# Kernel tuning notes

Measured on AMD Instinct MI355X. Metric: run time of the kernel, lower is better.

The kernel has to match this reference:

```python
import jax, jax.numpy as jnp
import numpy as np

L, H, DH, D, F, V, ENC, PAST = 8, 8, 128, 1024, 4096, 16384, 438, 447
MAXPOS = PAST + 1


def _ln(x, g, b):
    m = jnp.mean(x, -1, keepdims=True)
    v = jnp.mean((x - m) ** 2, -1, keepdims=True)
    return (x - m) * jax.lax.rsqrt(v + 1e-5) * g + b


def setup_inputs() -> dict:
    key = jax.random.key(0)
    ks = jax.random.split(key, 30)
    rn = lambda k, shape: jax.random.normal(k, shape, jnp.float32) * 0.02
    inp = {
        'input_ids': jax.random.randint(ks[0], (1, 1), 0, V, jnp.int32),
        'encoder_hidden_states': jax.random.normal(ks[1], (1, ENC, D), jnp.float32),
        'past_k': jax.random.normal(ks[2], (L, 1, H, PAST, DH), jnp.float32),
        'past_v': jax.random.normal(ks[3], (L, 1, H, PAST, DH), jnp.float32),
        'emb': rn(ks[4], (V, D)),
        'pos': rn(ks[5], (MAXPOS, D)),
        'ln1_g': jnp.ones((L, D), jnp.float32), 'ln1_b': jnp.zeros((L, D), jnp.float32),
        'wq_s': rn(ks[6], (L, D, D)), 'wk_s': rn(ks[7], (L, D, D)),
        'wv_s': rn(ks[8], (L, D, D)), 'wo_s': rn(ks[9], (L, D, D)),
        'ln2_g': jnp.ones((L, D), jnp.float32), 'ln2_b': jnp.zeros((L, D), jnp.float32),
        'wq_c': rn(ks[10], (L, D, D)), 'wk_c': rn(ks[11], (L, D, D)),
        'wv_c': rn(ks[12], (L, D, D)), 'wo_c': rn(ks[13], (L, D, D)),
        'ln3_g': jnp.ones((L, D), jnp.float32), 'ln3_b': jnp.zeros((L, D), jnp.float32),
        'w1': rn(ks[14], (L, D, F)), 'w2': rn(ks[15], (L, F, D)),
        'lnf_g': jnp.ones((D,), jnp.float32), 'lnf_b': jnp.zeros((D,), jnp.float32),
        'past_length': PAST,
    }
    return inp


def reference(input_ids, encoder_hidden_states, past_k, past_v, emb, pos,
              ln1_g, ln1_b, wq_s, wk_s, wv_s, wo_s,
              ln2_g, ln2_b, wq_c, wk_c, wv_c, wo_c,
              ln3_g, ln3_b, w1, w2, lnf_g, lnf_b, past_length):
    scale = 1.0 / np.sqrt(DH)
    # token embedding + learned position embedding at the current position
    x = emb[input_ids] + pos[past_length][None, None, :]  # (1,1,D)
    heads1 = lambda t: t.reshape(1, 1, H, DH).transpose(0, 2, 1, 3)      # (1,H,1,dh)
    for l in range(L):
        # --- self-attention over cached K/V + new token (pre-LN) ---
        h = _ln(x, ln1_g[l], ln1_b[l])
        q = heads1(h @ wq_s[l])
        k = heads1(h @ wk_s[l])
        v = heads1(h @ wv_s[l])
        K = jnp.concatenate([past_k[l], k], axis=2)   # (1,H,PAST+1,dh)
        Vv = jnp.concatenate([past_v[l], v], axis=2)
        a = jax.nn.softmax(jnp.einsum('bhqd,bhkd->bhqk', q, K) * scale, axis=-1)
        o = jnp.einsum('bhqk,bhkd->bhqd', a, Vv).transpose(0, 2, 1, 3).reshape(1, 1, D)
        x = x + o @ wo_s[l]
        # --- cross-attention to encoder states ---
        h = _ln(x, ln2_g[l], ln2_b[l])
        q = heads1(h @ wq_c[l])
        Kc = (encoder_hidden_states @ wk_c[l]).reshape(1, ENC, H, DH).transpose(0, 2, 1, 3)
        Vc = (encoder_hidden_states @ wv_c[l]).reshape(1, ENC, H, DH).transpose(0, 2, 1, 3)
        a = jax.nn.softmax(jnp.einsum('bhqd,bhkd->bhqk', q, Kc) * scale, axis=-1)
        o = jnp.einsum('bhqk,bhkd->bhqd', a, Vc).transpose(0, 2, 1, 3).reshape(1, 1, D)
        x = x + o @ wo_c[l]
        # --- FFN ---
        h = _ln(x, ln3_g[l], ln3_b[l])
        x = x + jax.nn.gelu(h @ w1[l]) @ w2[l]
    x = _ln(x, lnf_g, lnf_b)
    logits = x @ emb.T  # tied lm_head -> (1,1,V)
    return logits
```

## Files before the change

kernel.cpp:

```cpp
#include <hip/hip_runtime.h>
#include <hip/hip_bf16.h>

#define D 1024
#define Hh 8
#define DHd 128
#define Ff 4096
#define Ll 8
#define Vv 16384
#define ENCn 438
#define PASTn 447
#define NCH 7
#define SCALE 0.08838834764831845f

typedef __hip_bfloat16 bf16;
typedef __attribute__((ext_vector_type(8))) short short8;
typedef __attribute__((ext_vector_type(4))) float floatx4;

template<typename T> __device__ __forceinline__ float ldg_(const void* p, size_t i);
template<> __device__ __forceinline__ float ldg_<bf16>(const void* p, size_t i) {
    return __bfloat162float(((const bf16*)p)[i]);
}
template<> __device__ __forceinline__ float ldg_<float>(const void* p, size_t i) {
    return ((const float*)p)[i];
}
template<typename T> __device__ __forceinline__ void stg_(void* p, size_t i, float v);
template<> __device__ __forceinline__ void stg_<bf16>(void* p, size_t i, float v) {
    ((bf16*)p)[i] = __float2bfloat16(v);
}
template<> __device__ __forceinline__ void stg_<float>(void* p, size_t i, float v) {
    ((float*)p)[i] = v;
}

template<typename T> __device__ __forceinline__ void load8(const void* p, size_t i, float* o);
template<> __device__ __forceinline__ void load8<bf16>(const void* p, size_t i, float* o) {
    short8 v = *reinterpret_cast<const short8*>(reinterpret_cast<const short*>(p) + i);
#pragma unroll
    for (int k = 0; k < 8; k++)
        o[k] = __uint_as_float(((unsigned)(unsigned short)v[k]) << 16);
}
template<> __device__ __forceinline__ void load8<float>(const void* p, size_t i, float* o) {
    const floatx4* q = reinterpret_cast<const floatx4*>(reinterpret_cast<const float*>(p) + i);
    floatx4 a = q[0], b = q[1];
#pragma unroll
    for (int k = 0; k < 4; k++) { o[k] = a[k]; o[4 + k] = b[k]; }
}

__device__ __forceinline__ float blkmax(float v, float* sm) {
#pragma unroll
    for (int off = 32; off; off >>= 1) v = fmaxf(v, __shfl_xor(v, off));
    __syncthreads();
    if ((threadIdx.x & 63) == 0) sm[threadIdx.x >> 6] = v;
    __syncthreads();
    return fmaxf(fmaxf(sm[0], sm[1]), fmaxf(sm[2], sm[3]));
}
__device__ __forceinline__ float blksum(float v, float* sm) {
#pragma unroll
    for (int off = 32; off; off >>= 1) v += __shfl_xor(v, off);
    __syncthreads();
    if ((threadIdx.x & 63) == 0) sm[threadIdx.x >> 6] = v;
    __syncthreads();
    return sm[0] + sm[1] + sm[2] + sm[3];
}
__device__ __forceinline__ void blksum2(float a, float b, float* sm, float& oa, float& ob) {
#pragma unroll
    for (int off = 32; off; off >>= 1) { a += __shfl_xor(a, off); b += __shfl_xor(b, off); }
    __syncthreads();
    if ((threadIdx.x & 63) == 0) { int w = threadIdx.x >> 6; sm[w] = a; sm[4 + w] = b; }
    __syncthreads();
    oa = sm[0] + sm[1] + sm[2] + sm[3];
    ob = sm[4] + sm[5] + sm[6] + sm[7];
}

__device__ __forceinline__ float comb4(const float* P, int i) {
    return P[i] + P[1024 + i] + P[2048 + i] + P[3072 + i];
}

template<typename T, int NROWS>
__device__ __forceinline__ float mv_tile(const void* W, size_t base, int ldW,
                                         const float* xs, float* sm) {
    int c8 = threadIdx.x & 7, s = threadIdx.x >> 3;
    const int IT = NROWS / 32;
    float acc[8];
#pragma unroll
    for (int k = 0; k < 8; k++) acc[k] = 0.f;
    size_t idx = base + (size_t)(s * IT) * ldW + c8 * 8;
#pragma unroll 8
    for (int it = 0; it < IT; ++it) {
        float w8[8];
        load8<T>(W, idx, w8);
        float xv = xs[s * IT + it];
#pragma unroll
        for (int k = 0; k < 8; k++) acc[k] = fmaf(xv, w8[k], acc[k]);
        idx += (size_t)ldW;
    }
    __syncthreads();
#pragma unroll
    for (int k = 0; k < 8; k++) sm[s * 64 + c8 * 8 + k] = acc[k];
    __syncthreads();
    float y = 0.f;
    if (threadIdx.x < 64) {
#pragma unroll 8
        for (int s2 = 0; s2 < 32; s2++) y += sm[s2 * 64 + threadIdx.x];
    }
    return y;
}

template<typename T>
__device__ __forceinline__ void ln_slice(const float* Xp, const void* g, const void* b,
                                         size_t o1, int row0, float* xs, float* sm) {
    int t = threadIdx.x;
    float xv[4];
    float s = 0.f, sq = 0.f;
#pragma unroll
    for (int k = 0; k < 4; k++) {
        float v = comb4(Xp, t * 4 + k);
        xv[k] = v; s += v; sq += v * v;
    }
    float S, SQ;
    blksum2(s, sq, sm, S, SQ);
    float m = S * (1.f / D);
    float rstd = rsqrtf(SQ * (1.f / D) - m * m + 1e-5f);
#pragma unroll
    for (int k = 0; k < 4; k++) {
        int i = t * 4 + k;
        int rel = i - row0;
        if ((unsigned)rel < 256u)
            xs[rel] = (xv[k] - m) * rstd * ldg_<T>(g, o1 + i) + ldg_<T>(b, o1 + i);
    }
    __syncthreads();
}

__global__ void k_probe(const void* ones, int* flag) {
    if (threadIdx.x == 0)
        *flag = (*(const unsigned*)ones == 0x3F803F80u) ? 1 : 0;
}

template<typename T>
__device__ void embed_body(const int* ids, const int* plen, const void* emb,
                           const void* pos, float* XAp) {
    int t = threadIdx.x;
    int id = ids[0], pl = plen[0];
    for (int i = t; i < D; i += 256) {
        XAp[i] = ldg_<T>(emb, (size_t)id * D + i) + ldg_<T>(pos, (size_t)pl * D + i);
        XAp[1024 + i] = 0.f; XAp[2048 + i] = 0.f; XAp[3072 + i] = 0.f;
    }
}
__global__ __launch_bounds__(256) void k_embed(const int* flag, const int* ids,
                                               const int* plen, const void* emb,
                                               const void* pos, float* XAp) {
    if (*flag) embed_body<bf16>(ids, plen, emb, pos, XAp);
    else       embed_body<float>(ids, plen, emb, pos, XAp);
}

template<typename T>
__device__ void qkv_body(const float* XAp, const void* g, const void* b, size_t o1,
                         const void* W0, const void* W1, const void* W2, size_t o2,
                         float* qp, float* kp, float* vp, float* xs, float* sm) {
    int bid = blockIdx.x;
    int mat = bid >> 6, rem = bid & 63;
    int cb = rem >> 2, rc = rem & 3;
    int j0 = cb * 64, row0 = rc * 256;
    ln_slice<T>(XAp, g, b, o1, row0, xs, sm);
    const void* W = (mat == 0) ? W0 : ((mat == 1) ? W1 : W2);
    float* out = (mat == 0) ? qp : ((mat == 1) ? kp : vp);
    float y = mv_tile<T, 256>(W, o2 + (size_t)row0 * D + j0, D, xs, sm);
    if (threadIdx.x < 64) out[rc * 1024 + j0 + threadIdx.x] = y;
}
__global__ __launch_bounds__(256) void k_qkv(const int* flag,
    const float* XAp, const void* g, const void* b, size_t o1,
    const void* W0, const void* W1, const void* W2, size_t o2,
    float* qp, float* kp, float* vp) {
    __shared__ float xs[256];
    __shared__ float sm[2048];
    if (*flag) qkv_body<bf16>(XAp, g, b, o1, W0, W1, W2, o2, qp, kp, vp, xs, sm);
    else       qkv_body<float>(XAp, g, b, o1, W0, W1, W2, o2, qp, kp, vp, xs, sm);
}

template<typename T>
__device__ void attn_body(const float* qp, const float* kp, const float* vp,
                          const void* pk, const void* pv, size_t kvo,
                          float* pm, float* plv, float* pacc,
                          float* qsh, float* knl, float* vnl, float* sc, float* sm) {
    int h = blockIdx.x / NCH, cc = blockIdx.x % NCH;
    int t = threadIdx.x;
    if (t < 128) {
        qsh[t] = comb4(qp, h * 128 + t);
        if (cc == NCH - 1) vnl[t] = comb4(vp, h * 128 + t);
    } else if (cc == NCH - 1) {
        int d = t - 128;
        knl[d] = comb4(kp, h * 128 + d);
    }
    __syncthreads();
    int kk = t >> 2, part = t & 3;
    int p = cc * 64 + kk;
    float acc = 0.f;
    if (p < PASTn) {
        size_t base = kvo + ((size_t)h * PASTn + p) * DHd + part * 32;
#pragma unroll
        for (int w = 0; w < 4; w++) {
            float k8[8]; load8<T>(pk, base + w * 8, k8);
#pragma unroll
            for (int j = 0; j < 8; j++) acc = fmaf(qsh[part * 32 + w * 8 + j], k8[j], acc);
        }
    } else {
#pragma unroll 8
        for (int j = 0; j < 32; j++) acc += qsh[part * 32 + j] * knl[part * 32 + j];
    }
    acc += __shfl_xor(acc, 1);
    acc += __shfl_xor(acc, 2);
    if (part == 0) sc[kk] = acc * SCALE;
    __syncthreads();
    float v0 = (t < 64) ? sc[t] : -1e30f;
    float M = blkmax(v0, sm);
    float e = (t < 64) ? expf(sc[t] - M) : 0.f;
    if (t < 64) sc[t] = e;
    float lsum = blksum(e, sm);
    int dv = t & 15, kg = t >> 4;
    float a8[8];
#pragma unroll
    for (int k = 0; k < 8; k++) a8[k] = 0.f;
#pragma unroll
    for (int q4 = 0; q4 < 4; q4++) {
        int k2 = kg + q4 * 16;
        int p2 = cc * 64 + k2;
        float pw = sc[k2];
        if (p2 < PASTn) {
            float v8[8];
            load8<T>(pv, kvo + ((size_t)h * PASTn + p2) * DHd + dv * 8, v8);
#pragma unroll
            for (int j = 0; j < 8; j++) a8[j] = fmaf(pw, v8[j], a8[j]);
        } else {
#pragma unroll
            for (int j = 0; j < 8; j++) a8[j] = fmaf(pw, vnl[dv * 8 + j], a8[j]);
        }
    }
    __syncthreads();
#pragma unroll
    for (int j = 0; j < 8; j++) sm[kg * 128 + dv * 8 + j] = a8[j];
    __syncthreads();
    if (t < 128) {
        float s = 0.f;
#pragma unroll 4
        for (int g2 = 0; g2 < 16; g2++) s += sm[g2 * 128 + t];
        pacc[((size_t)h * NCH + cc) * 128 + t] = s;
    }
    if (t == 0) { pm[h * 8 + cc] = M; plv[h * 8 + cc] = lsum; }
}
__global__ __launch_bounds__(256) void k_attn(const int* flag,
    const float* qp, const float* kp, const float* vp,
    const void* pk, const void* pv, size_t kvo,
    float* pm, float* plv, float* pacc) {
    __shared__ float qsh[128], knl[128], vnl[128], sc[64];
    __shared__ float sm[2048];
    if (*flag) attn_body<bf16>(qp, kp, vp, pk, pv, kvo, pm, plv, pacc, qsh, knl, vnl, sc, sm);
    else       attn_body<float>(qp, kp, vp, pk, pv, kvo, pm, plv, pacc, qsh, knl, vnl, sc, sm);
}

template<typename T>
__device__ void combwo_body(const float* pm, const float* plv, const float* pacc,
                            const void* W, size_t o2, const float* XAp, float* XBp,
                            float* fac, float* xs, float* sm) {
    int cb = blockIdx.x >> 2, rc = blockIdx.x & 3;
    int j0 = cb * 64, row0 = rc * 256;
    int t = threadIdx.x;
    if (t < Hh) {
        float M = -1e30f;
        for (int c = 0; c < NCH; c++) M = fmaxf(M, pm[t * 8 + c]);
        float fs[NCH]; float den = 0.f;
        for (int c = 0; c < NCH; c++) { fs[c] = expf(pm[t * 8 + c] - M); den += fs[c] * plv[t * 8 + c]; }
        float inv = 1.f / den;
        for (int c = 0; c < NCH; c++) fac[t * NCH + c] = fs[c] * inv;
    }
    __syncthreads();
    int hd = row0 + t;
    int h = hd >> 7, d = hd & 127;
    float o = 0.f;
#pragma unroll
    for (int c = 0; c < NCH; c++) o += fac[h * NCH + c] * pacc[((size_t)h * NCH + c) * 128 + d];
    xs[t] = o;
    __syncthreads();
    float y = mv_tile<T, 256>(W, o2 + (size_t)row0 * D + j0, D, xs, sm);
    if (t < 64) {
        float r = (rc == 0) ? comb4(XAp, j0 + t) : 0.f;
        XBp[rc * 1024 + j0 + t] = y + r;
    }
}
__global__ __launch_bounds__(256) void k_combwo(const int* flag,
    const float* pm, const float* plv, const float* pacc,
    const void* W, size_t o2, const float* XAp, float* XBp) {
    __shared__ float fac[Hh * NCH];
    __shared__ float xs[256];
    __shared__ float sm[2048];
    if (*flag) combwo_body<bf16>(pm, plv, pacc, W, o2, XAp, XBp, fac, xs, sm);
    else       combwo_body<float>(pm, plv, pacc, W, o2, XAp, XBp, fac, xs, sm);
}

template<typename T>
__device__ void lnmv_body(const float* Xp, const void* g, const void* b, size_t o1,
                          const void* W, size_t wo, int ldW, float* outp,
                          float* xs, float* sm) {
    int cb = blockIdx.x >> 2, rc = blockIdx.x & 3;
    int j0 = cb * 64, row0 = rc * 256;
    ln_slice<T>(Xp, g, b, o1, row0, xs, sm);
    float y = mv_tile<T, 256>(W, wo + (size_t)row0 * ldW + j0, ldW, xs, sm);
    if (threadIdx.x < 64) outp[(size_t)rc * ldW + j0 + threadIdx.x] = y;
}
__global__ __launch_bounds__(256) void k_lnmv(const int* flag,
    const float* Xp, const void* g, const void* b, size_t o1,
    const void* W, size_t wo, int ldW, float* outp) {
    __shared__ float xs[256];
    __shared__ float sm[2048];
    if (*flag) lnmv_body<bf16>(Xp, g, b, o1, W, wo, ldW, outp, xs, sm);
    else       lnmv_body<float>(Xp, g, b, o1, W, wo, ldW, outp, xs, sm);
}

template<typename T>
__device__ void tvec_body(const float* qcp, const void* Wk, size_t o2, float* tv, float* qsl) {
    int h = blockIdx.x >> 3, dc = blockIdx.x & 7;
    int t = threadIdx.x;
    if (t < 128) qsl[t] = comb4(qcp, h * 128 + t);
    __syncthreads();
    int out = t >> 1, half = t & 1;
    int d = dc * 128 + out;
    size_t base = o2 + (size_t)d * D + h * 128 + half * 64;
    float acc = 0.f;
#pragma unroll
    for (int w = 0; w < 8; w++) {
        float w8[8]; load8<T>(Wk, base + w * 8, w8);
#pragma unroll
        for (int j = 0; j < 8; j++) acc = fmaf(qsl[half * 64 + w * 8 + j], w8[j], acc);
    }
    acc += __shfl_xor(acc, 1);
    if (half == 0) tv[(size_t)h * D + d] = acc * SCALE;
}
__global__ __launch_bounds__(256) void k_tvec(const int* flag, const float* qcp,
                                              const void* Wk, size_t o2, float* tv) {
    __shared__ float qsl[128];
    if (*flag) tvec_body<bf16>(qcp, Wk, o2, tv, qsl);
    else       tvec_body<float>(qcp, Wk, o2, tv, qsl);
}

template<typename T>
__device__ void cscore_body(const void* enc, const float* tv, float* scb, float* tsh) {
    int h = blockIdx.x / 14, rcw = blockIdx.x % 14;
    int t = threadIdx.x;
#pragma unroll
    for (int k = 0; k < 4; k++) tsh[t * 4 + k] = tv[(size_t)h * D + t * 4 + k];
    __syncthreads();
    int rr = t >> 3, part = t & 7;
    int r = rcw * 32 + rr;
    float acc = 0.f;
    if (r < ENCn) {
        size_t base = (size_t)r * D + part * 128;
#pragma unroll 8
        for (int w = 0; w < 16; w++) {
            float e8[8]; load8<T>(enc, base + w * 8, e8);
#pragma unroll
            for (int j = 0; j < 8; j++) acc = fmaf(tsh[part * 128 + w * 8 + j], e8[j], acc);
        }
    }
    acc += __shfl_xor(acc, 1);
    acc += __shfl_xor(acc, 2);
    acc += __shfl_xor(acc, 4);
    if (part == 0 && r < ENCn) scb[h * 448 + r] = acc;
}
__global__ __launch_bounds__(256) void k_cscore(const int* flag, const void* enc,
                                                const float* tv, float* scb) {
    __shared__ float tsh[D];
    if (*flag) cscore_body<bf16>(enc, tv, scb, tsh);
    else       cscore_body<float>(enc, tv, scb, tsh);
}

template<typename T>
__device__ void softw_body(const float* scb, const void* enc, float* wvb,
                           float* p, float* sm) {
    int h = blockIdx.x >> 3, dc = blockIdx.x & 7;
    int t = threadIdx.x;
    float v1 = (t < ENCn) ? scb[h * 448 + t] : -1e30f;
    float v2 = (256 + t < ENCn) ? scb[h * 448 + 256 + t] : -1e30f;
    float M = blkmax(fmaxf(v1, v2), sm);
    float e1 = (t < ENCn) ? expf(v1 - M) : 0.f;
    float e2 = (256 + t < ENCn) ? expf(v2 - M) : 0.f;
    p[t] = e1;
    if (t + 256 < 448) p[t + 256] = e2;
    float inv = 1.f / blksum(e1 + e2, sm);
    int dv = t & 15, rg = t >> 4;
    float a8[8];
#pragma unroll
    for (int k = 0; k < 8; k++) a8[k] = 0.f;
    for (int r = rg; r < ENCn; r += 16) {
        float e8[8]; load8<T>(enc, (size_t)r * D + dc * 128 + dv * 8, e8);
        float pw = p[r];
#pragma unroll
        for (int j = 0; j < 8; j++) a8[j] = fmaf(pw, e8[j], a8[j]);
    }
    __syncthreads();
#pragma unroll
    for (int j = 0; j < 8; j++) sm[rg * 128 + dv * 8 + j] = a8[j];
    __syncthreads();
    if (t < 128) {
        float s = 0.f;
#pragma unroll 4
        for (int g2 = 0; g2 < 16; g2++) s += sm[g2 * 128 + t];
        wvb[(size_t)h * D + dc * 128 + t] = s * inv;
    }
}
__global__ __launch_bounds__(256) void k_softw(const int* flag, const float* scb,
                                               const void* enc, float* wvb) {
    __shared__ float p[448];
    __shared__ float sm[2048];
    if (*flag) softw_body<bf16>(scb, enc, wvb, p, sm);
    else       softw_body<float>(scb, enc, wvb, p, sm);
}

template<typename T>
__device__ void ovec_body(const float* wvb, const void* Wv, size_t o2, float* ocp,
                          float* xs, float* sm) {
    int cb = blockIdx.x >> 2, rc = blockIdx.x & 3;
    int j0 = cb * 64, row0 = rc * 256;
    int h = j0 >> 7;
    int t = threadIdx.x;
    xs[t] = wvb[(size_t)h * D + row0 + t];
    __syncthreads();
    float y = mv_tile<T, 256>(Wv, o2 + (size_t)row0 * D + j0, D, xs, sm);
    if (t < 64) ocp[rc * 1024 + j0 + t] = y;
}
__global__ __launch_bounds__(256) void k_ovec(const int* flag, const float* wvb,
                                              const void* Wv, size_t o2, float* ocp) {
    __shared__ float xs[256];
    __shared__ float sm[2048];
    if (*flag) ovec_body<bf16>(wvb, Wv, o2, ocp, xs, sm);
    else       ovec_body<float>(wvb, Wv, o2, ocp, xs, sm);
}

template<typename T>
__device__ void woc_body(const float* ocp, const void* W, size_t o2,
                         const float* XBp, float* XCp, float* xs, float* sm) {
    int cb = blockIdx.x >> 2, rc = blockIdx.x & 3;
    int j0 = cb * 64, row0 = rc * 256;
    int t = threadIdx.x;
    xs[t] = comb4(ocp, row0 + t);
    __syncthreads();
    float y = mv_tile<T, 256>(W, o2 + (size_t)row0 * D + j0, D, xs, sm);
    if (t < 64) {
        float r = (rc == 0) ? comb4(XBp, j0 + t) : 0.f;
        XCp[rc * 1024 + j0 + t] = y + r;
    }
}
__global__ __launch_bounds__(256) void k_woc(const int* flag, const float* ocp,
    const void* W, size_t o2, const float* XBp, float* XCp) {
    __shared__ float xs[256];
    __shared__ float sm[2048];
    if (*flag) woc_body<bf16>(ocp, W, o2, XBp, XCp, xs, sm);
    else       woc_body<float>(ocp, W, o2, XBp, XCp, xs, sm);
}

template<typename T>
__device__ void w2_body(const float* ubp, const void* W, size_t oG,
                        const float* XCp, float* XAp, float* xs, float* sm) {
    int cb = blockIdx.x >> 2, rc = blockIdx.x & 3;
    int j0 = cb * 64, row0 = rc * 1024;
    int t = threadIdx.x;
#pragma unroll
    for (int k = 0; k < 4; k++) {
        int i = t * 4 + k;
        int gi = row0 + i;
        float u = ubp[gi] + ubp[4096 + gi] + ubp[8192 + gi] + ubp[12288 + gi];
        float g2 = 0.7978845608028654f * (u + 0.044715f * u * u * u);
        xs[i] = 0.5f * u * (1.f + tanhf(g2));
    }
    __syncthreads();
    float y = mv_tile<T, 1024>(W, oG + (size_t)row0 * D + j0, D, xs, sm);
    if (t < 64) {
        float r = (rc == 0) ? comb4(XCp, j0 + t) : 0.f;
        XAp[rc * 1024 + j0 + t] = y + r;
    }
}
__global__ __launch_bounds__(256) void k_w2(const int* flag, const float* ubp,
    const void* W, size_t oG, const float* XCp, float* XAp) {
    __shared__ float xs[1024];
    __shared__ float sm[2048];
    if (*flag) w2_body<bf16>(ubp, W, oG, XCp, XAp, xs, sm);
    else       w2_body<float>(ubp, W, oG, XCp, XAp, xs, sm);
}

template<typename T>
__device__ void logits_body(const float* XAp, const void* g, const void* b,
                            const void* emb, void* out, float* hsh, float* sm) {
    int t = threadIdx.x;
    float xv[4];
    float s = 0.f, sq = 0.f;
#pragma unroll
    for (int k = 0; k < 4; k++) {
        float v = comb4(XAp, t * 4 + k);
        xv[k] = v; s += v; sq += v * v;
    }
    float S, SQ;
    blksum2(s, sq, sm, S, SQ);
    float m = S * (1.f / D);
    float rstd = rsqrtf(SQ * (1.f / D) - m * m + 1e-5f);
#pragma unroll
    for (int k = 0; k < 4; k++) {
        int i = t * 4 + k;
        hsh[i] = (xv[k] - m) * rstd * ldg_<T>(g, i) + ldg_<T>(b, i);
    }
    __syncthreads();
    int v = blockIdx.x * 64 + (t >> 2), part = t & 3;
    size_t base = (size_t)v * D + part * 256;
    float acc = 0.f;
#pragma unroll 8
    for (int w = 0; w < 32; w++) {
        float e8[8]; load8<T>(emb, base + w * 8, e8);
#pragma unroll
        for (int j = 0; j < 8; j++) acc = fmaf(hsh[part * 256 + w * 8 + j], e8[j], acc);
    }
    acc += __shfl_xor(acc, 1);
    acc += __shfl_xor(acc, 2);
    if (part == 0) stg_<T>(out, v, acc);
}
__global__ __launch_bounds__(256) void k_logits(const int* flag, const float* XAp,
                                                const void* g, const void* b,
                                                const void* emb, void* out) {
    __shared__ float hsh[D];
    __shared__ float sm[8];
    if (*flag) logits_body<bf16>(XAp, g, b, emb, out, hsh, sm);
    else       logits_body<float>(XAp, g, b, emb, out, hsh, sm);
}

extern "C" void kernel_launch(void* const* d_in, const int* in_sizes, int n_in,
                              void* d_out, int out_size, void* d_ws, size_t ws_size,
                              hipStream_t stream) {
    const int*  ids    = (const int*)d_in[0];
    const void* enc    = d_in[1];
    const void* past_k = d_in[2];
    const void* past_v = d_in[3];
    const void* emb    = d_in[4];
    const void* pos    = d_in[5];
    const void* ln1_g  = d_in[6];
    const void* ln1_b  = d_in[7];
    const void* wq_s   = d_in[8];
    const void* wk_s   = d_in[9];
    const void* wv_s   = d_in[10];
    const void* wo_s   = d_in[11];
    const void* ln2_g  = d_in[12];
    const void* ln2_b  = d_in[13];
    const void* wq_c   = d_in[14];
    const void* wk_c   = d_in[15];
    const void* wv_c   = d_in[16];
    const void* wo_c   = d_in[17];
    const void* ln3_g  = d_in[18];
    const void* ln3_b  = d_in[19];
    const void* w1     = d_in[20];
    const void* w2     = d_in[21];
    const void* lnf_g  = d_in[22];
    const void* lnf_b  = d_in[23];
    const int*  plen   = (const int*)d_in[24];

    float* ws   = (float*)d_ws;
    float* XAp  = ws;
    float* XBp  = ws + 4096;
    float* XCp  = ws + 8192;
    float* qp   = ws + 12288;
    float* kp   = ws + 16384;
    float* vp   = ws + 20480;
    float* qcp  = ws + 24576;
    float* ocp  = ws + 28672;
    float* pm   = ws + 32768;
    float* plv  = ws + 32832;
    float* pacc = ws + 32896;
    float* tv   = ws + 40064;
    float* scb  = ws + 48256;
    float* wvb  = ws + 51840;
    float* ubp  = ws + 60032;
    int*   flag = (int*)(ws + 76416);

    k_probe<<<1, 64, 0, stream>>>(ln1_g, flag);
    k_embed<<<1, 256, 0, stream>>>(flag, ids, plen, emb, pos, XAp);

    for (int l = 0; l < Ll; l++) {
        size_t o1  = (size_t)l * D;
        size_t o2  = (size_t)l * D * D;
        size_t oF  = (size_t)l * D * Ff;
        size_t oG  = (size_t)l * Ff * D;
        size_t oKV = (size_t)l * Hh * PASTn * DHd;

        k_qkv<<<192, 256, 0, stream>>>(flag, XAp, ln1_g, ln1_b, o1,
                                       wq_s, wk_s, wv_s, o2, qp, kp, vp);
        k_attn<<<56, 256, 0, stream>>>(flag, qp, kp, vp, past_k, past_v, oKV,
                                       pm, plv, pacc);
        k_combwo<<<64, 256, 0, stream>>>(flag, pm, plv, pacc, wo_s, o2, XAp, XBp);
        k_lnmv<<<64, 256, 0, stream>>>(flag, XBp, ln2_g, ln2_b, o1,
                                       wq_c, o2, D, qcp);
        k_tvec<<<64, 256, 0, stream>>>(flag, qcp, wk_c, o2, tv);
        k_cscore<<<112, 256, 0, stream>>>(flag, enc, tv, scb);
        k_softw<<<64, 256, 0, stream>>>(flag, scb, enc, wvb);
        k_ovec<<<64, 256, 0, stream>>>(flag, wvb, wv_c, o2, ocp);
        k_woc<<<64, 256, 0, stream>>>(flag, ocp, wo_c, o2, XBp, XCp);
        k_lnmv<<<256, 256, 0, stream>>>(flag, XCp, ln3_g, ln3_b, o1,
                                        w1, oF, Ff, ubp);
        k_w2<<<64, 256, 0, stream>>>(flag, ubp, w2, oG, XCp, XAp);
    }

    k_logits<<<256, 256, 0, stream>>>(flag, XAp, lnf_g, lnf_b, emb, d_out);
}
```

Before: 988.4 us.

## Fuse all decoder stages into one persistent kernel with grid barriers

Replaces roughly 90 separate kernel launches with a single persistent 256-block kernel. The stages are separated by a hierarchical atomic grid barrier, and partial matvec sums are accumulated with atomicAdd into zero-initialised buffers. GELU is folded into the W2 stage, and the stage tilings are reshaped so every stage uses 256 blocks. The aim is to remove launch overhead and the per-kernel tail, at the cost of software barriers. The barrier has a spin limit that breaks out, and it relies on all 256 blocks being co-resident, which is a deadlock or correctness risk.

```diff
diff --git a/kernel.cpp b/kernel.cpp
--- a/kernel.cpp
+++ b/kernel.cpp
@@ -16,6 +16,24 @@
 typedef __attribute__((ext_vector_type(8))) short short8;
 typedef __attribute__((ext_vector_type(4))) float floatx4;
 
+#define WS_XD    0
+#define WS_XBD   1024
+#define WS_ACCA  2048
+#define WS_ACCB  3072
+#define WS_ACCC  4096
+#define WS_QKV   5120
+#define WS_QC    8192
+#define WS_OC    9216
+#define WS_TV    10240
+#define WS_SCB   18432
+#define WS_WVB   22016
+#define WS_UB    30208
+#define WS_PACC  34304
+#define WS_PM    41472
+#define WS_PLV   41536
+#define WS_BAR   41600
+#define WS_FLAG  41632
+
 template<typename T> __device__ __forceinline__ float ldg_(const void* p, size_t i);
 template<> __device__ __forceinline__ float ldg_<bf16>(const void* p, size_t i) {
     return __bfloat162float(((const bf16*)p)[i]);
@@ -30,7 +48,6 @@
 template<> __device__ __forceinline__ void stg_<float>(void* p, size_t i, float v) {
     ((float*)p)[i] = v;
 }
-
 template<typename T> __device__ __forceinline__ void load8(const void* p, size_t i, float* o);
 template<> __device__ __forceinline__ void load8<bf16>(const void* p, size_t i, float* o) {
     short8 v = *reinterpret_cast<const short8*>(reinterpret_cast<const short*>(p) + i);
@@ -45,6 +62,11 @@
     for (int k = 0; k < 4; k++) { o[k] = a[k]; o[4 + k] = b[k]; }
 }
 
+__device__ __forceinline__ float gelu_(float u) {
+    float g = 0.7978845608028654f * (u + 0.044715f * u * u * u);
+    return 0.5f * u * (1.f + tanhf(g));
+}
+
 __device__ __forceinline__ float blkmax(float v, float* sm) {
 #pragma unroll
     for (int off = 32; off; off >>= 1) v = fmaxf(v, __shfl_xor(v, off));
@@ -71,8 +93,29 @@
     ob = sm[4] + sm[5] + sm[6] + sm[7];
 }
 
-__device__ __forceinline__ float comb4(const float* P, int i) {
-    return P[i] + P[1024 + i] + P[2048 + i] + P[3072 + i];
+__device__ __forceinline__ void gbar(int* bar, int& phase, int bid) {
+    __syncthreads();
+    phase++;
+    if (threadIdx.x == 0) {
+        __threadfence();
+        int v = __hip_atomic_fetch_add(&bar[bid & 15], 1, __ATOMIC_RELAXED,
+                                       __HIP_MEMORY_SCOPE_AGENT);
+        if (v == phase * 16 - 1) {
+            int r = __hip_atomic_fetch_add(&bar[16], 1, __ATOMIC_RELAXED,
+                                           __HIP_MEMORY_SCOPE_AGENT);
+            if (r == phase * 16 - 1)
+                __hip_atomic_store(&bar[17], phase, __ATOMIC_RELEASE,
+                                   __HIP_MEMORY_SCOPE_AGENT);
+        }
+        int spins = 0;
+        while (__hip_atomic_load(&bar[17], __ATOMIC_ACQUIRE,
+                                 __HIP_MEMORY_SCOPE_AGENT) < phase) {
+            __builtin_amdgcn_s_sleep(2);
+            if (++spins > 200000) break;
+        }
+        __threadfence();
+    }
+    __syncthreads();
 }
 
 template<typename T, int NROWS>
@@ -84,7 +127,7 @@
 #pragma unroll
     for (int k = 0; k < 8; k++) acc[k] = 0.f;
     size_t idx = base + (size_t)(s * IT) * ldW + c8 * 8;
-#pragma unroll 8
+#pragma unroll
     for (int it = 0; it < IT; ++it) {
         float w8[8];
         load8<T>(W, idx, w8);
@@ -99,21 +142,25 @@
     __syncthreads();
     float y = 0.f;
     if (threadIdx.x < 64) {
-#pragma unroll 8
+#pragma unroll
         for (int s2 = 0; s2 < 32; s2++) y += sm[s2 * 64 + threadIdx.x];
     }
     return y;
 }
 
-template<typename T>
-__device__ __forceinline__ void ln_slice(const float* Xp, const void* g, const void* b,
-                                         size_t o1, int row0, float* xs, float* sm) {
+template<typename T, int NT, int RL>
+__device__ __forceinline__ float ln_mv(const float* A, const float* B2, const float* C2,
+                                       const void* g, const void* bb, size_t o1, int row0,
+                                       const void* W, size_t wbase, int ldW,
+                                       float* xs, float* sm) {
     int t = threadIdx.x;
-    float xv[4];
-    float s = 0.f, sq = 0.f;
+    float xv[4], s = 0.f, sq = 0.f;
 #pragma unroll
     for (int k = 0; k < 4; k++) {
-        float v = comb4(Xp, t * 4 + k);
+        int i = t * 4 + k;
+        float v = A[i];
+        if (NT > 1) v += B2[i];
+        if (NT > 2) v += C2[i];
         xv[k] = v; s += v; sq += v * v;
     }
     float S, SQ;
@@ -124,407 +171,385 @@
     for (int k = 0; k < 4; k++) {
         int i = t * 4 + k;
         int rel = i - row0;
-        if ((unsigned)rel < 256u)
-            xs[rel] = (xv[k] - m) * rstd * ldg_<T>(g, o1 + i) + ldg_<T>(b, o1 + i);
-    }
-    __syncthreads();
-}
-
-__global__ void k_probe(const void* ones, int* flag) {
-    if (threadIdx.x == 0)
-        *flag = (*(const unsigned*)ones == 0x3F803F80u) ? 1 : 0;
+        if ((unsigned)rel < (unsigned)RL)
+            xs[rel] = (xv[k] - m) * rstd * ldg_<T>(g, o1 + i) + ldg_<T>(bb, o1 + i);
+    }
+    __syncthreads();
+    return mv_tile<T, RL>(W, wbase, ldW, xs, sm);
+}
+
+__global__ void k_init(const void* ones, float* ws) {
+    int t = threadIdx.x;
+    for (int i = WS_ACCA + t; i < WS_QKV + 3072; i += 256) ws[i] = 0.f;
+    int* bar = (int*)(ws + WS_BAR);
+    if (t < 32) bar[t] = 0;
+    if (t == 0)
+        ((int*)(ws + WS_FLAG))[0] = (*(const unsigned*)ones == 0x3F803F80u) ? 1 : 0;
 }
 
 template<typename T>
-__device__ void embed_body(const int* ids, const int* plen, const void* emb,
-                           const void* pos, float* XAp) {
-    int t = threadIdx.x;
-    int id = ids[0], pl = plen[0];
-    for (int i = t; i < D; i += 256) {
-        XAp[i] = ldg_<T>(emb, (size_t)id * D + i) + ldg_<T>(pos, (size_t)pl * D + i);
-        XAp[1024 + i] = 0.f; XAp[2048 + i] = 0.f; XAp[3072 + i] = 0.f;
-    }
-}
-__global__ __launch_bounds__(256) void k_embed(const int* flag, const int* ids,
-                                               const int* plen, const void* emb,
-                                               const void* pos, float* XAp) {
-    if (*flag) embed_body<bf16>(ids, plen, emb, pos, XAp);
-    else       embed_body<float>(ids, plen, emb, pos, XAp);
-}
-
-template<typename T>
-__device__ void qkv_body(const float* XAp, const void* g, const void* b, size_t o1,
-                         const void* W0, const void* W1, const void* W2, size_t o2,
-                         float* qp, float* kp, float* vp, float* xs, float* sm) {
-    int bid = blockIdx.x;
-    int mat = bid >> 6, rem = bid & 63;
-    int cb = rem >> 2, rc = rem & 3;
-    int j0 = cb * 64, row0 = rc * 256;
-    ln_slice<T>(XAp, g, b, o1, row0, xs, sm);
-    const void* W = (mat == 0) ? W0 : ((mat == 1) ? W1 : W2);
-    float* out = (mat == 0) ? qp : ((mat == 1) ? kp : vp);
-    float y = mv_tile<T, 256>(W, o2 + (size_t)row0 * D + j0, D, xs, sm);
-    if (threadIdx.x < 64) out[rc * 1024 + j0 + threadIdx.x] = y;
-}
-__global__ __launch_bounds__(256) void k_qkv(const int* flag,
-    const float* XAp, const void* g, const void* b, size_t o1,
-    const void* W0, const void* W1, const void* W2, size_t o2,
-    float* qp, float* kp, float* vp) {
-    __shared__ float xs[256];
-    __shared__ float sm[2048];
-    if (*flag) qkv_body<bf16>(XAp, g, b, o1, W0, W1, W2, o2, qp, kp, vp, xs, sm);
-    else       qkv_body<float>(XAp, g, b, o1, W0, W1, W2, o2, qp, kp, vp, xs, sm);
-}
-
-template<typename T>
-__device__ void attn_body(const float* qp, const float* kp, const float* vp,
-                          const void* pk, const void* pv, size_t kvo,
-                          float* pm, float* plv, float* pacc,
-                          float* qsh, float* knl, float* vnl, float* sc, float* sm) {
-    int h = blockIdx.x / NCH, cc = blockIdx.x % NCH;
-    int t = threadIdx.x;
-    if (t < 128) {
-        qsh[t] = comb4(qp, h * 128 + t);
-        if (cc == NCH - 1) vnl[t] = comb4(vp, h * 128 + t);
-    } else if (cc == NCH - 1) {
-        int d = t - 128;
-        knl[d] = comb4(kp, h * 128 + d);
-    }
-    __syncthreads();
-    int kk = t >> 2, part = t & 3;
-    int p = cc * 64 + kk;
-    float acc = 0.f;
-    if (p < PASTn) {
-        size_t base = kvo + ((size_t)h * PASTn + p) * DHd + part * 32;
-#pragma unroll
-        for (int w = 0; w < 4; w++) {
-            float k8[8]; load8<T>(pk, base + w * 8, k8);
-#pragma unroll
-            for (int j = 0; j < 8; j++) acc = fmaf(qsh[part * 32 + w * 8 + j], k8[j], acc);
-        }
-    } else {
-#pragma unroll 8
-        for (int j = 0; j < 32; j++) acc += qsh[part * 32 + j] * knl[part * 32 + j];
-    }
-    acc += __shfl_xor(acc, 1);
-    acc += __shfl_xor(acc, 2);
-    if (part == 0) sc[kk] = acc * SCALE;
-    __syncthreads();
-    float v0 = (t < 64) ? sc[t] : -1e30f;
-    float M = blkmax(v0, sm);
-    float e = (t < 64) ? expf(sc[t] - M) : 0.f;
-    if (t < 64) sc[t] = e;
-    float lsum = blksum(e, sm);
-    int dv = t & 15, kg = t >> 4;
-    float a8[8];
-#pragma unroll
-    for (int k = 0; k < 8; k++) a8[k] = 0.f;
-#pragma unroll
-    for (int q4 = 0; q4 < 4; q4++) {
-        int k2 = kg + q4 * 16;
-        int p2 = cc * 64 + k2;
-        float pw = sc[k2];
-        if (p2 < PASTn) {
-            float v8[8];
-            load8<T>(pv, kvo + ((size_t)h * PASTn + p2) * DHd + dv * 8, v8);
-#pragma unroll
-            for (int j = 0; j < 8; j++) a8[j] = fmaf(pw, v8[j], a8[j]);
-        } else {
-#pragma unroll
-            for (int j = 0; j < 8; j++) a8[j] = fmaf(pw, vnl[dv * 8 + j], a8[j]);
-        }
-    }
-    __syncthreads();
-#pragma unroll
-    for (int j = 0; j < 8; j++) sm[kg * 128 + dv * 8 + j] = a8[j];
-    __syncthreads();
-    if (t < 128) {
-        float s = 0.f;
-#pragma unroll 4
-        for (int g2 = 0; g2 < 16; g2++) s += sm[g2 * 128 + t];
-        pacc[((size_t)h * NCH + cc) * 128 + t] = s;
-    }
-    if (t == 0) { pm[h * 8 + cc] = M; plv[h * 8 + cc] = lsum; }
-}
-__global__ __launch_bounds__(256) void k_attn(const int* flag,
-    const float* qp, const float* kp, const float* vp,
-    const void* pk, const void* pv, size_t kvo,
-    float* pm, float* plv, float* pacc) {
-    __shared__ float qsh[128], knl[128], vnl[128], sc[64];
-    __shared__ float sm[2048];
-    if (*flag) attn_body<bf16>(qp, kp, vp, pk, pv, kvo, pm, plv, pacc, qsh, knl, vnl, sc, sm);
-    else       attn_body<float>(qp, kp, vp, pk, pv, kvo, pm, plv, pacc, qsh, knl, vnl, sc, sm);
-}
-
-template<typename T>
-__device__ void combwo_body(const float* pm, const float* plv, const float* pacc,
-                            const void* W, size_t o2, const float* XAp, float* XBp,
-                            float* fac, float* xs, float* sm) {
-    int cb = blockIdx.x >> 2, rc = blockIdx.x & 3;
-    int j0 = cb * 64, row0 = rc * 256;
-    int t = threadIdx.x;
-    if (t < Hh) {
-        float M = -1e30f;
-        for (int c = 0; c < NCH; c++) M = fmaxf(M, pm[t * 8 + c]);
-        float fs[NCH]; float den = 0.f;
-        for (int c = 0; c < NCH; c++) { fs[c] = expf(pm[t * 8 + c] - M); den += fs[c] * plv[t * 8 + c]; }
-        float inv = 1.f / den;
-        for (int c = 0; c < NCH; c++) fac[t * NCH + c] = fs[c] * inv;
-    }
-    __syncthreads();
-    int hd = row0 + t;
-    int h = hd >> 7, d = hd & 127;
-    float o = 0.f;
-#pragma unroll
-    for (int c = 0; c < NCH; c++) o += fac[h * NCH + c] * pacc[((size_t)h * NCH + c) * 128 + d];
-    xs[t] = o;
-    __syncthreads();
-    float y = mv_tile<T, 256>(W, o2 + (size_t)row0 * D + j0, D, xs, sm);
-    if (t < 64) {
-        float r = (rc == 0) ? comb4(XAp, j0 + t) : 0.f;
-        XBp[rc * 1024 + j0 + t] = y + r;
-    }
-}
-__global__ __launch_bounds__(256) void k_combwo(const int* flag,
-    const float* pm, const float* plv, const float* pacc,
-    const void* W, size_t o2, const float* XAp, float* XBp) {
-    __shared__ float fac[Hh * NCH];
-    __shared__ float xs[256];
-    __shared__ float sm[2048];
-    if (*flag) combwo_body<bf16>(pm, plv, pacc, W, o2, XAp, XBp, fac, xs, sm);
-    else       combwo_body<float>(pm, plv, pacc, W, o2, XAp, XBp, fac, xs, sm);
-}
-
-template<typename T>
-__device__ void lnmv_body(const float* Xp, const void* g, const void* b, size_t o1,
-                          const void* W, size_t wo, int ldW, float* outp,
-                          float* xs, float* sm) {
-    int cb = blockIdx.x >> 2, rc = blockIdx.x & 3;
-    int j0 = cb * 64, row0 = rc * 256;
-    ln_slice<T>(Xp, g, b, o1, row0, xs, sm);
-    float y = mv_tile<T, 256>(W, wo + (size_t)row0 * ldW + j0, ldW, xs, sm);
-    if (threadIdx.x < 64) outp[(size_t)rc * ldW + j0 + threadIdx.x] = y;
-}
-__global__ __launch_bounds__(256) void k_lnmv(const int* flag,
-    const float* Xp, const void* g, const void* b, size_t o1,
-    const void* W, size_t wo, int ldW, float* outp) {
-    __shared__ float xs[256];
-    __shared__ float sm[2048];
-    if (*flag) lnmv_body<bf16>(Xp, g, b, o1, W, wo, ldW, outp, xs, sm);
-    else       lnmv_body<float>(Xp, g, b, o1, W, wo, ldW, outp, xs, sm);
-}
-
-template<typename T>
-__device__ void tvec_body(const float* qcp, const void* Wk, size_t o2, float* tv, float* qsl) {
-    int h = blockIdx.x >> 3, dc = blockIdx.x & 7;
-    int t = threadIdx.x;
-    if (t < 128) qsl[t] = comb4(qcp, h * 128 + t);
-    __syncthreads();
-    int out = t >> 1, half = t & 1;
-    int d = dc * 128 + out;
-    size_t base = o2 + (size_t)d * D + h * 128 + half * 64;
-    float acc = 0.f;
-#pragma unroll
-    for (int w = 0; w < 8; w++) {
-        float w8[8]; load8<T>(Wk, base + w * 8, w8);
-#pragma unroll
-        for (int j = 0; j < 8; j++) acc = fmaf(qsl[half * 64 + w * 8 + j], w8[j], acc);
-    }
-    acc += __shfl_xor(acc, 1);
-    if (half == 0) tv[(size_t)h * D + d] = acc * SCALE;
-}
-__global__ __launch_bounds__(256) void k_tvec(const int* flag, const float* qcp,
-                                              const void* Wk, size_t o2, float* tv) {
-    __shared__ float qsl[128];
-    if (*flag) tvec_body<bf16>(qcp, Wk, o2, tv, qsl);
-    else       tvec_body<float>(qcp, Wk, o2, tv, qsl);
-}
-
-template<typename T>
-__device__ void cscore_body(const void* enc, const float* tv, float* scb, float* tsh) {
-    int h = blockIdx.x / 14, rcw = blockIdx.x % 14;
-    int t = threadIdx.x;
-#pragma unroll
-    for (int k = 0; k < 4; k++) tsh[t * 4 + k] = tv[(size_t)h * D + t * 4 + k];
-    __syncthreads();
-    int rr = t >> 3, part = t & 7;
-    int r = rcw * 32 + rr;
-    float acc = 0.f;
-    if (r < ENCn) {
-        size_t base = (size_t)r * D + part * 128;
-#pragma unroll 8
-        for (int w = 0; w < 16; w++) {
-            float e8[8]; load8<T>(enc, base + w * 8, e8);
-#pragma unroll
-            for (int j = 0; j < 8; j++) acc = fmaf(tsh[part * 128 + w * 8 + j], e8[j], acc);
-        }
-    }
-    acc += __shfl_xor(acc, 1);
-    acc += __shfl_xor(acc, 2);
-    acc += __shfl_xor(acc, 4);
-    if (part == 0 && r < ENCn) scb[h * 448 + r] = acc;
-}
-__global__ __launch_bounds__(256) void k_cscore(const int* flag, const void* enc,
-                                                const float* tv, float* scb) {
-    __shared__ float tsh[D];
-    if (*flag) cscore_body<bf16>(enc, tv, scb, tsh);
-    else       cscore_body<float>(enc, tv, scb, tsh);
-}
-
-template<typename T>
-__device__ void softw_body(const float* scb, const void* enc, float* wvb,
-                           float* p, float* sm) {
-    int h = blockIdx.x >> 3, dc = blockIdx.x & 7;
-    int t = threadIdx.x;
-    float v1 = (t < ENCn) ? scb[h * 448 + t] : -1e30f;
-    float v2 = (256 + t < ENCn) ? scb[h * 448 + 256 + t] : -1e30f;
-    float M = blkmax(fmaxf(v1, v2), sm);
-    float e1 = (t < ENCn) ? expf(v1 - M) : 0.f;
-    float e2 = (256 + t < ENCn) ? expf(v2 - M) : 0.f;
-    p[t] = e1;
-    if (t + 256 < 448) p[t + 256] = e2;
-    float inv = 1.f / blksum(e1 + e2, sm);
-    int dv = t & 15, rg = t >> 4;
-    float a8[8];
-#pragma unroll
-    for (int k = 0; k < 8; k++) a8[k] = 0.f;
-    for (int r = rg; r < ENCn; r += 16) {
-        float e8[8]; load8<T>(enc, (size_t)r * D + dc * 128 + dv * 8, e8);
-        float pw = p[r];
-#pragma unroll
-        for (int j = 0; j < 8; j++) a8[j] = fmaf(pw, e8[j], a8[j]);
-    }
-    __syncthreads();
-#pragma unroll
-    for (int j = 0; j < 8; j++) sm[rg * 128 + dv * 8 + j] = a8[j];
-    __syncthreads();
-    if (t < 128) {
-        float s = 0.f;
-#pragma unroll 4
-        for (int g2 = 0; g2 < 16; g2++) s += sm[g2 * 128 + t];
-        wvb[(size_t)h * D + dc * 128 + t] = s * inv;
-    }
-}
-__global__ __launch_bounds__(256) void k_softw(const int* flag, const float* scb,
-                                               const void* enc, float* wvb) {
-    __shared__ float p[448];
-    __shared__ float sm[2048];
-    if (*flag) softw_body<bf16>(scb, enc, wvb, p, sm);
-    else       softw_body<float>(scb, enc, wvb, p, sm);
-}
-
-template<typename T>
-__device__ void ovec_body(const float* wvb, const void* Wv, size_t o2, float* ocp,
-                          float* xs, float* sm) {
-    int cb = blockIdx.x >> 2, rc = blockIdx.x & 3;
-    int j0 = cb * 64, row0 = rc * 256;
-    int h = j0 >> 7;
-    int t = threadIdx.x;
-    xs[t] = wvb[(size_t)h * D + row0 + t];
-    __syncthreads();
-    float y = mv_tile<T, 256>(Wv, o2 + (size_t)row0 * D + j0, D, xs, sm);
-    if (t < 64) ocp[rc * 1024 + j0 + t] = y;
-}
-__global__ __launch_bounds__(256) void k_ovec(const int* flag, const float* wvb,
-                                              const void* Wv, size_t o2, float* ocp) {
-    __shared__ float xs[256];
-    __shared__ float sm[2048];
-    if (*flag) ovec_body<bf16>(wvb, Wv, o2, ocp, xs, sm);
-    else       ovec_body<float>(wvb, Wv, o2, ocp, xs, sm);
-}
-
-template<typename T>
-__device__ void woc_body(const float* ocp, const void* W, size_t o2,
-                         const float* XBp, float* XCp, float* xs, float* sm) {
-    int cb = blockIdx.x >> 2, rc = blockIdx.x & 3;
-    int j0 = cb * 64, row0 = rc * 256;
-    int t = threadIdx.x;
-    xs[t] = comb4(ocp, row0 + t);
-    __syncthreads();
-    float y = mv_tile<T, 256>(W, o2 + (size_t)row0 * D + j0, D, xs, sm);
-    if (t < 64) {
-        float r = (rc == 0) ? comb4(XBp, j0 + t) : 0.f;
-        XCp[rc * 1024 + j0 + t] = y + r;
-    }
-}
-__global__ __launch_bounds__(256) void k_woc(const int* flag, const float* ocp,
-    const void* W, size_t o2, const float* XBp, float* XCp) {
-    __shared__ float xs[256];
-    __shared__ float sm[2048];
-    if (*flag) woc_body<bf16>(ocp, W, o2, XBp, XCp, xs, sm);
-    else       woc_body<float>(ocp, W, o2, XBp, XCp, xs, sm);
-}
-
-template<typename T>
-__device__ void w2_body(const float* ubp, const void* W, size_t oG,
-                        const float* XCp, float* XAp, float* xs, float* sm) {
-    int cb = blockIdx.x >> 2, rc = blockIdx.x & 3;
-    int j0 = cb * 64, row0 = rc * 1024;
-    int t = threadIdx.x;
-#pragma unroll
-    for (int k = 0; k < 4; k++) {
-        int i = t * 4 + k;
-        int gi = row0 + i;
-        float u = ubp[gi] + ubp[4096 + gi] + ubp[8192 + gi] + ubp[12288 + gi];
-        float g2 = 0.7978845608028654f * (u + 0.044715f * u * u * u);
-        xs[i] = 0.5f * u * (1.f + tanhf(g2));
-    }
-    __syncthreads();
-    float y = mv_tile<T, 1024>(W, oG + (size_t)row0 * D + j0, D, xs, sm);
-    if (t < 64) {
-        float r = (rc == 0) ? comb4(XCp, j0 + t) : 0.f;
-        XAp[rc * 1024 + j0 + t] = y + r;
-    }
-}
-__global__ __launch_bounds__(256) void k_w2(const int* flag, const float* ubp,
-    const void* W, size_t oG, const float* XCp, float* XAp) {
+__device__ void mega(const int* ids, const void* enc, const void* pk, const void* pv,
+                     const void* emb, const void* pos,
+                     const void* ln1g, const void* ln1b,
+                     const void* wqs, const void* wks, const void* wvs, const void* wos,
+                     const void* ln2g, const void* ln2b,
+                     const void* wqc, const void* wkc, const void* wvc, const void* woc_,
+                     const void* ln3g, const void* ln3b,
+                     const void* w1p, const void* w2p,
+                     const void* lnfg, const void* lnfb, const int* plen,
+                     void* out, float* ws, float* xs, float* sm, float* aux) {
+    const int bid = blockIdx.x, t = threadIdx.x;
+    float* Xd   = ws + WS_XD;
+    float* XBd  = ws + WS_XBD;
+    float* accA = ws + WS_ACCA;
+    float* accB = ws + WS_ACCB;
+    float* accC = ws + WS_ACCC;
+    float* qkvd = ws + WS_QKV;
+    float* qc   = ws + WS_QC;
+    float* ocb  = ws + WS_OC;
+    float* tv   = ws + WS_TV;
+    float* scb  = ws + WS_SCB;
+    float* wvb  = ws + WS_WVB;
+    float* ub   = ws + WS_UB;
+    float* pacc = ws + WS_PACC;
+    float* pm   = ws + WS_PM;
+    float* plv  = ws + WS_PLV;
+    int*   bar  = (int*)(ws + WS_BAR);
+    int phase = 0;
+
+    if (bid == 0) {
+        int id = ids[0], pl = plen[0];
+        for (int i = t; i < D; i += 256)
+            XBd[i] = ldg_<T>(emb, (size_t)id * D + i) + ldg_<T>(pos, (size_t)pl * D + i);
+    }
+    gbar(bar, phase, bid);
+
+#pragma unroll 1
+    for (int l = 0; l < Ll; l++) {
+        size_t o1  = (size_t)l * D;
+        size_t o2  = (size_t)l * D * D;
+        size_t oF  = (size_t)l * D * Ff;
+        size_t oG  = (size_t)l * Ff * D;
+        size_t oKV = (size_t)l * Hh * PASTn * DHd;
+
+        if (bid < 192) {
+            int mat = bid >> 6, rem = bid & 63, cb = rem >> 2, rc = rem & 3;
+            int j0 = cb * 64, row0 = rc * 256;
+            const void* W = (mat == 0) ? wqs : ((mat == 1) ? wks : wvs);
+            float y = ln_mv<T, 3, 256>(XBd, accC, accA, ln1g, ln1b, o1, row0,
+                                       W, o2 + (size_t)row0 * D + j0, D, xs, sm);
+            if (t < 64) atomicAdd(&qkvd[mat * 1024 + j0 + t], y);
+        } else if (bid < 196) {
+            int i = (bid - 192) * 256 + t;
+            Xd[i] = XBd[i] + accC[i] + accA[i];
+        } else if (bid < 200) {
+            ocb[(bid - 196) * 256 + t] = 0.f;
+        }
+        gbar(bar, phase, bid);
+
+        if (bid < 56) {
+            float* qsh = aux;
+            float* knl = aux + 128;
+            float* vnl = aux + 256;
+            float* sc  = aux + 384;
+            int h = bid / NCH, cc = bid % NCH;
+            if (t < 128) {
+                qsh[t] = qkvd[h * 128 + t];
+                if (cc == NCH - 1) vnl[t] = qkvd[2048 + h * 128 + t];
+            } else if (cc == NCH - 1) {
+                knl[t - 128] = qkvd[1024 + h * 128 + (t - 128)];
+            }
+            __syncthreads();
+            int kk = t >> 2, part = t & 3;
+            int p = cc * 64 + kk;
+            float acc = 0.f;
+            if (p < PASTn) {
+                size_t base = oKV + ((size_t)h * PASTn + p) * DHd + part * 32;
+#pragma unroll
+                for (int w = 0; w < 4; w++) {
+                    float k8[8]; load8<T>(pk, base + w * 8, k8);
+#pragma unroll
+                    for (int j = 0; j < 8; j++)
+                        acc = fmaf(qsh[part * 32 + w * 8 + j], k8[j], acc);
+                }
+            } else {
+#pragma unroll
+                for (int j = 0; j < 32; j++)
+                    acc += qsh[part * 32 + j] * knl[part * 32 + j];
+            }
+            acc += __shfl_xor(acc, 1);
+            acc += __shfl_xor(acc, 2);
+            if (part == 0) sc[kk] = acc * SCALE;
+            __syncthreads();
+            float v0 = (t < 64) ? sc[t] : -1e30f;
+            float M = blkmax(v0, sm);
+            float e = (t < 64) ? expf(sc[t] - M) : 0.f;
+            if (t < 64) sc[t] = e;
+            float lsum = blksum(e, sm);
+            int dv = t & 15, kg = t >> 4;
+            float a8[8];
+#pragma unroll
+            for (int k = 0; k < 8; k++) a8[k] = 0.f;
+#pragma unroll
+            for (int q4 = 0; q4 < 4; q4++) {
+                int k2 = kg + q4 * 16;
+                int p2 = cc * 64 + k2;
+                float pw = sc[k2];
+                if (p2 < PASTn) {
+                    float v8[8];
+                    load8<T>(pv, oKV + ((size_t)h * PASTn + p2) * DHd + dv * 8, v8);
+#pragma unroll
+                    for (int j = 0; j < 8; j++) a8[j] = fmaf(pw, v8[j], a8[j]);
+                } else {
+#pragma unroll
+                    for (int j = 0; j < 8; j++) a8[j] = fmaf(pw, vnl[dv * 8 + j], a8[j]);
+                }
+            }
+            __syncthreads();
+#pragma unroll
+            for (int j = 0; j < 8; j++) sm[kg * 128 + dv * 8 + j] = a8[j];
+            __syncthreads();
+            if (t < 128) {
+                float s = 0.f;
+#pragma unroll
+                for (int g2 = 0; g2 < 16; g2++) s += sm[g2 * 128 + t];
+                pacc[((size_t)h * NCH + cc) * 128 + t] = s;
+            }
+            if (t == 0) { pm[h * 8 + cc] = M; plv[h * 8 + cc] = lsum; }
+        } else if (bid < 60) {
+            accC[(bid - 56) * 256 + t] = 0.f;
+        } else if (bid < 64) {
+            qc[(bid - 60) * 256 + t] = 0.f;
+        }
+        gbar(bar, phase, bid);
+
+        {
+            int cb = bid >> 4, rc = bid & 15;
+            int j0 = cb * 64, row0 = rc * 64;
+            if (t < Hh) {
+                float M = -1e30f;
+                for (int c = 0; c < NCH; c++) M = fmaxf(M, pm[t * 8 + c]);
+                float fs[NCH]; float den = 0.f;
+                for (int c = 0; c < NCH; c++) {
+                    fs[c] = expf(pm[t * 8 + c] - M);
+                    den += fs[c] * plv[t * 8 + c];
+                }
+                float inv = 1.f / den;
+                for (int c = 0; c < NCH; c++) aux[t * NCH + c] = fs[c] * inv;
+            }
+            __syncthreads();
+            if (t < 64) {
+                int row = row0 + t;
+                int h = row >> 7, d = row & 127;
+                float o = 0.f;
+#pragma unroll
+                for (int c = 0; c < NCH; c++)
+                    o += aux[h * NCH + c] * pacc[((size_t)h * NCH + c) * 128 + d];
+                xs[t] = o;
+            }
+            __syncthreads();
+            float y = mv_tile<T, 64>(wos, o2 + (size_t)row0 * D + j0, D, xs, sm);
+            if (t < 64) atomicAdd(&accB[j0 + t], y);
+        }
+        gbar(bar, phase, bid);
+
+        {
+            int cb = bid >> 4, rc = bid & 15;
+            int j0 = cb * 64, row0 = rc * 64;
+            float y = ln_mv<T, 2, 64>(Xd, accB, accB, ln2g, ln2b, o1, row0,
+                                      wqc, o2 + (size_t)row0 * D + j0, D, xs, sm);
+            if (t < 64) atomicAdd(&qc[j0 + t], y);
+        }
+        gbar(bar, phase, bid);
+
+        if (bid < 64) {
+            int h = bid >> 3, dc = bid & 7;
+            if (t < 128) xs[t] = qc[h * 128 + t];
+            __syncthreads();
+            int o = t >> 1, half = t & 1;
+            int d = dc * 128 + o;
+            size_t base = o2 + (size_t)d * D + h * 128 + half * 64;
+            float acc = 0.f;
+#pragma unroll
+            for (int w = 0; w < 8; w++) {
+                float w8[8]; load8<T>(wkc, base + w * 8, w8);
+#pragma unroll
+                for (int j = 0; j < 8; j++)
+                    acc = fmaf(xs[half * 64 + w * 8 + j], w8[j], acc);
+            }
+            acc += __shfl_xor(acc, 1);
+            if (half == 0) tv[(size_t)h * D + d] = acc * SCALE;
+        } else if (bid < 68) {
+            accA[(bid - 64) * 256 + t] = 0.f;
+        } else if (bid < 72) {
+            int i = (bid - 68) * 256 + t;
+            XBd[i] = Xd[i] + accB[i];
+        }
+        gbar(bar, phase, bid);
+
+        if (bid < 112) {
+            int h = bid / 14, rcw = bid % 14;
+#pragma unroll
+            for (int k = 0; k < 4; k++) xs[t * 4 + k] = tv[(size_t)h * D + t * 4 + k];
+            __syncthreads();
+            int rr = t >> 3, part = t & 7;
+            int r = rcw * 32 + rr;
+            float acc = 0.f;
+            if (r < ENCn) {
+                size_t base = (size_t)r * D + part * 128;
+#pragma unroll
+                for (int w = 0; w < 16; w++) {
+                    float e8[8]; load8<T>(enc, base + w * 8, e8);
+#pragma unroll
+                    for (int j = 0; j < 8; j++)
+                        acc = fmaf(xs[part * 128 + w * 8 + j], e8[j], acc);
+                }
+            }
+            acc += __shfl_xor(acc, 1);
+            acc += __shfl_xor(acc, 2);
+            acc += __shfl_xor(acc, 4);
+            if (part == 0 && r < ENCn) scb[h * 448 + r] = acc;
+        } else if (bid < 116) {
+            accB[(bid - 112) * 256 + t] = 0.f;
+        }
+        gbar(bar, phase, bid);
+
+        if (bid < 64) {
+            float* p = aux;
+            int h = bid >> 3, dc = bid & 7;
+            float v1 = (t < ENCn) ? scb[h * 448 + t] : -1e30f;
+            float v2 = (256 + t < ENCn) ? scb[h * 448 + 256 + t] : -1e30f;
+            float M = blkmax(fmaxf(v1, v2), sm);
+            float e1 = (t < ENCn) ? expf(v1 - M) : 0.f;
+            float e2 = (256 + t < ENCn) ? expf(v2 - M) : 0.f;
+            p[t] = e1;
+            if (t + 256 < 448) p[t + 256] = e2;
+            float inv = 1.f / blksum(e1 + e2, sm);
+            int dv = t & 15, rg = t >> 4;
+            float a8[8];
+#pragma unroll
+            for (int k = 0; k < 8; k++) a8[k] = 0.f;
+            for (int r = rg; r < ENCn; r += 16) {
+                float e8[8]; load8<T>(enc, (size_t)r * D + dc * 128 + dv * 8, e8);
+                float pw = p[r];
+#pragma unroll
+                for (int j = 0; j < 8; j++) a8[j] = fmaf(pw, e8[j], a8[j]);
+            }
+            __syncthreads();
+#pragma unroll
+            for (int j = 0; j < 8; j++) sm[rg * 128 + dv * 8 + j] = a8[j];
+            __syncthreads();
+            if (t < 128) {
+                float s = 0.f;
+#pragma unroll
+                for (int g2 = 0; g2 < 16; g2++) s += sm[g2 * 128 + t];
+                wvb[(size_t)h * D + dc * 128 + t] = s * inv;
+            }
+        } else if (bid < 76) {
+            qkvd[(bid - 64) * 256 + t] = 0.f;
+        } else if (bid < 92) {
+            ub[(bid - 76) * 256 + t] = 0.f;
+        }
+        gbar(bar, phase, bid);
+
+        {
+            int cb = bid >> 4, rc = bid & 15;
+            int j0 = cb * 64, row0 = rc * 64;
+            int h = j0 >> 7;
+            if (t < 64) xs[t] = wvb[(size_t)h * D + row0 + t];
+            __syncthreads();
+            float y = mv_tile<T, 64>(wvc, o2 + (size_t)row0 * D + j0, D, xs, sm);
+            if (t < 64) atomicAdd(&ocb[j0 + t], y);
+        }
+        gbar(bar, phase, bid);
+
+        {
+            int cb = bid >> 4, rc = bid & 15;
+            int j0 = cb * 64, row0 = rc * 64;
+            if (t < 64) xs[t] = ocb[row0 + t];
+            __syncthreads();
+            float y = mv_tile<T, 64>(woc_, o2 + (size_t)row0 * D + j0, D, xs, sm);
+            if (t < 64) atomicAdd(&accC[j0 + t], y);
+        }
+        gbar(bar, phase, bid);
+
+        {
+            int cb = bid >> 2, rc = bid & 3;
+            int j0 = cb * 64, row0 = rc * 256;
+            float y = ln_mv<T, 2, 256>(XBd, accC, accC, ln3g, ln3b, o1, row0,
+                                       w1p, oF + (size_t)row0 * Ff + j0, Ff, xs, sm);
+            if (t < 64) atomicAdd(&ub[j0 + t], y);
+        }
+        gbar(bar, phase, bid);
+
+        {
+            int cb = bid >> 4, rc = bid & 15;
+            int j0 = cb * 64, row0 = rc * 256;
+            xs[t] = gelu_(ub[row0 + t]);
+            __syncthreads();
+            float y = mv_tile<T, 256>(w2p, oG + (size_t)row0 * D + j0, D, xs, sm);
+            if (t < 64) atomicAdd(&accA[j0 + t], y);
+        }
+        gbar(bar, phase, bid);
+    }
+
+    {
+        float xv[4], s = 0.f, sq = 0.f;
+#pragma unroll
+        for (int k = 0; k < 4; k++) {
+            int i = t * 4 + k;
+            float v = XBd[i] + accC[i] + accA[i];
+            xv[k] = v; s += v; sq += v * v;
+        }
+        float S, SQ;
+        blksum2(s, sq, sm, S, SQ);
+        float m = S * (1.f / D);
+        float rstd = rsqrtf(SQ * (1.f / D) - m * m + 1e-5f);
+#pragma unroll
+        for (int k = 0; k < 4; k++) {
+            int i = t * 4 + k;
+            xs[i] = (xv[k] - m) * rstd * ldg_<T>(lnfg, i) + ldg_<T>(lnfb, i);
+        }
+        __syncthreads();
+        int v = bid * 64 + (t >> 2), part = t & 3;
+        size_t base = (size_t)v * D + part * 256;
+        float acc = 0.f;
+#pragma unroll
+        for (int w = 0; w < 32; w++) {
+            float e8[8]; load8<T>(emb, base + w * 8, e8);
+#pragma unroll
+            for (int j = 0; j < 8; j++)
+                acc = fmaf(xs[part * 256 + w * 8 + j], e8[j], acc);
+        }
+        acc += __shfl_xor(acc, 1);
+        acc += __shfl_xor(acc, 2);
+        if (part == 0) stg_<T>(out, v, acc);
+    }
+}
+
+__global__ __launch_bounds__(256, 2) void k_mega(
+    const int* ids, const void* enc, const void* pk, const void* pv,
+    const void* emb, const void* pos,
+    const void* ln1g, const void* ln1b,
+    const void* wqs, const void* wks, const void* wvs, const void* wos,
+    const void* ln2g, const void* ln2b,
+    const void* wqc, const void* wkc, const void* wvc, const void* woc_,
+    const void* ln3g, const void* ln3b,
+    const void* w1p, const void* w2p,
+    const void* lnfg, const void* lnfb, const int* plen,
+    void* out, float* ws) {
     __shared__ float xs[1024];
     __shared__ float sm[2048];
-    if (*flag) w2_body<bf16>(ubp, W, oG, XCp, XAp, xs, sm);
-    else       w2_body<float>(ubp, W, oG, XCp, XAp, xs, sm);
-}
-
-template<typename T>
-__device__ void logits_body(const float* XAp, const void* g, const void* b,
-                            const void* emb, void* out, float* hsh, float* sm) {
-    int t = threadIdx.x;
-    float xv[4];
-    float s = 0.f, sq = 0.f;
-#pragma unroll
-    for (int k = 0; k < 4; k++) {
-        float v = comb4(XAp, t * 4 + k);
-        xv[k] = v; s += v; sq += v * v;
-    }
-    float S, SQ;
-    blksum2(s, sq, sm, S, SQ);
-    float m = S * (1.f / D);
-    float rstd = rsqrtf(SQ * (1.f / D) - m * m + 1e-5f);
-#pragma unroll
-    for (int k = 0; k < 4; k++) {
-        int i = t * 4 + k;
-        hsh[i] = (xv[k] - m) * rstd * ldg_<T>(g, i) + ldg_<T>(b, i);
-    }
-    __syncthreads();
-    int v = blockIdx.x * 64 + (t >> 2), part = t & 3;
-    size_t base = (size_t)v * D + part * 256;
-    float acc = 0.f;
-#pragma unroll 8
-    for (int w = 0; w < 32; w++) {
-        float e8[8]; load8<T>(emb, base + w * 8, e8);
-#pragma unroll
-        for (int j = 0; j < 8; j++) acc = fmaf(hsh[part * 256 + w * 8 + j], e8[j], acc);
-    }
-    acc += __shfl_xor(acc, 1);
-    acc += __shfl_xor(acc, 2);
-    if (part == 0) stg_<T>(out, v, acc);
-}
-__global__ __launch_bounds__(256) void k_logits(const int* flag, const float* XAp,
-                                                const void* g, const void* b,
-                                                const void* emb, void* out) {
-    __shared__ float hsh[D];
-    __shared__ float sm[8];
-    if (*flag) logits_body<bf16>(XAp, g, b, emb, out, hsh, sm);
-    else       logits_body<float>(XAp, g, b, emb, out, hsh, sm);
+    __shared__ float aux[512];
+    int flag = ((const int*)(ws + WS_FLAG))[0];
+    if (flag)
+        mega<bf16>(ids, enc, pk, pv, emb, pos, ln1g, ln1b, wqs, wks, wvs, wos,
+                   ln2g, ln2b, wqc, wkc, wvc, woc_, ln3g, ln3b, w1p, w2p,
+                   lnfg, lnfb, plen, out, ws, xs, sm, aux);
+    else
+        mega<float>(ids, enc, pk, pv, emb, pos, ln1g, ln1b, wqs, wks, wvs, wos,
+                    ln2g, ln2b, wqc, wkc, wvc, woc_, ln3g, ln3b, w1p, w2p,
+                    lnfg, lnfb, plen, out, ws, xs, sm, aux);
 }
 
 extern "C" void kernel_launch(void* const* d_in, const int* in_sizes, int n_in,
@@ -556,50 +581,12 @@
     const void* lnf_b  = d_in[23];
     const int*  plen   = (const int*)d_in[24];
 
-    float* ws   = (float*)d_ws;
-    float* XAp  = ws;
-    float* XBp  = ws + 4096;
-    float* XCp  = ws + 8192;
-    float* qp   = ws + 12288;
-    float* kp   = ws + 16384;
-    float* vp   = ws + 20480;
-    float* qcp  = ws + 24576;
-    float* ocp  = ws + 28672;
-    float* pm   = ws + 32768;
-    float* plv  = ws + 32832;
-    float* pacc = ws + 32896;
-    float* tv   = ws + 40064;
-    float* scb  = ws + 48256;
-    float* wvb  = ws + 51840;
-    float* ubp  = ws + 60032;
-    int*   flag = (int*)(ws + 76416);
-
-    k_probe<<<1, 64, 0, stream>>>(ln1_g, flag);
-    k_embed<<<1, 256, 0, stream>>>(flag, ids, plen, emb, pos, XAp);
-
-    for (int l = 0; l < Ll; l++) {
-        size_t o1  = (size_t)l * D;
-        size_t o2  = (size_t)l * D * D;
-        size_t oF  = (size_t)l * D * Ff;
-        size_t oG  = (size_t)l * Ff * D;
-        size_t oKV = (size_t)l * Hh * PASTn * DHd;
-
-        k_qkv<<<192, 256, 0, stream>>>(flag, XAp, ln1_g, ln1_b, o1,
-                                       wq_s, wk_s, wv_s, o2, qp, kp, vp);
-        k_attn<<<56, 256, 0, stream>>>(flag, qp, kp, vp, past_k, past_v, oKV,
-                                       pm, plv, pacc);
-        k_combwo<<<64, 256, 0, stream>>>(flag, pm, plv, pacc, wo_s, o2, XAp, XBp);
-        k_lnmv<<<64, 256, 0, stream>>>(flag, XBp, ln2_g, ln2_b, o1,
-                                       wq_c, o2, D, qcp);
-        k_tvec<<<64, 256, 0, stream>>>(flag, qcp, wk_c, o2, tv);
-        k_cscore<<<112, 256, 0, stream>>>(flag, enc, tv, scb);
-        k_softw<<<64, 256, 0, stream>>>(flag, scb, enc, wvb);
-        k_ovec<<<64, 256, 0, stream>>>(flag, wvb, wv_c, o2, ocp);
-        k_woc<<<64, 256, 0, stream>>>(flag, ocp, wo_c, o2, XBp, XCp);
-        k_lnmv<<<256, 256, 0, stream>>>(flag, XCp, ln3_g, ln3_b, o1,
-                                        w1, oF, Ff, ubp);
-        k_w2<<<64, 256, 0, stream>>>(flag, ubp, w2, oG, XCp, XAp);
-    }
-
-    k_logits<<<256, 256, 0, stream>>>(flag, XAp, lnf_g, lnf_b, emb, d_out);
-}
+    float* ws = (float*)d_ws;
+
+    k_init<<<1, 256, 0, stream>>>(ln1_g, ws);
+    k_mega<<<256, 256, 0, stream>>>(ids, enc, past_k, past_v, emb, pos,
+                                    ln1_g, ln1_b, wq_s, wk_s, wv_s, wo_s,
+                                    ln2_g, ln2_b, wq_c, wk_c, wv_c, wo_c,
+                                    ln3_g, ln3_b, w1, w2, lnf_g, lnf_b, plen,
+                                    d_out, ws);
+}
```

After: 3.188 ms. +222.5%, slower.
